# Optimization experiments

Measured on AMD Instinct MI355X. Metric: run time of the kernel, lower is better.

The kernel has to match this reference:

```python
import jax, jax.numpy as jnp
import numpy as np

# norse LIF/LI defaults
DT = 1e-3
TAU_SYN_INV = 200.0
TAU_MEM_INV = 100.0
V_TH = 1.0
V_LEAK = 0.0
V_RESET = 0.0
ALPHA = 100.0  # SuperSpike surrogate slope ('super' method)
N_CLASSES = 10


@jax.custom_vjp
def spike(x):
    # heaviside forward, SuperSpike surrogate backward
    return (x > 0).astype(x.dtype)

def _spike_fwd(x):
    return spike(x), x

def _spike_bwd(x, g):
    return (g / (ALPHA * jnp.abs(x) + 1.0) ** 2,)

spike.defvjp(_spike_fwd, _spike_bwd)


def conv2d(x, w, b):
    y = jax.lax.conv_general_dilated(x, w, (1, 1), 'VALID',
                                     dimension_numbers=('NCHW', 'OIHW', 'NCHW'))
    return y + b[None, :, None, None]


def maxpool2(x):
    return jax.lax.reduce_window(x, -jnp.inf, jax.lax.max,
                                 (1, 1, 2, 2), (1, 1, 2, 2), 'VALID')


def lif_step(inp, v, i):
    # norse lif_feed_forward_step
    v_dec = v + DT * TAU_MEM_INV * ((V_LEAK - v) + i)
    i_dec = i * (1.0 - DT * TAU_SYN_INV)
    z = spike(v_dec - V_TH)
    v_new = (1.0 - z) * v_dec + z * V_RESET
    i_new = i_dec + inp
    return z, v_new, i_new


def setup_inputs() -> dict:
    key = jax.random.key(0)
    ks = jax.random.split(key, 9)
    T, B, C, H = 32, 32, 1, 64
    feats = 13 * 13 * 32  # 5408
    return {
        'x': jax.random.normal(ks[0], (T, B, C, H, H), jnp.float32),
        'conv1_w': jax.random.normal(ks[1], (16, 1, 5, 5), jnp.float32) * 0.2,
        'conv1_b': jax.random.normal(ks[2], (16,), jnp.float32) * 0.1,
        'conv2_w': jax.random.normal(ks[3], (32, 16, 5, 5), jnp.float32) * 0.05,
        'conv2_b': jax.random.normal(ks[4], (32,), jnp.float32) * 0.1,
        'fc1_w': jax.random.normal(ks[5], (500, feats), jnp.float32) * 0.02,
        'fc1_b': jax.random.normal(ks[6], (500,), jnp.float32) * 0.1,
        'out_w': jax.random.normal(ks[7], (10, 500), jnp.float32) * 0.06,
    }


def reference(x, conv1_w, conv1_b, conv2_w, conv2_b, fc1_w, fc1_b, out_w):
    B = x.shape[1]
    zeros = lambda s: jnp.zeros(s, x.dtype)
    init = ((zeros((B, 16, 60, 60)), zeros((B, 16, 60, 60))),
            (zeros((B, 32, 26, 26)), zeros((B, 32, 26, 26))),
            (zeros((B, 500)), zeros((B, 500))),
            (zeros((B, N_CLASSES)), zeros((B, N_CLASSES))))

    def step(state, xt):
        (v0, i0), (v1, i1), (v2, i2), (vo, io) = state
        z = conv2d(xt, conv1_w, conv1_b)                     # [B,16,60,60]
        z, v0, i0 = lif_step(z, v0, i0)
        z = maxpool2(z)                                      # [B,16,30,30]
        z = N_CLASSES * conv2d(z, conv2_w, conv2_b)          # [B,32,26,26]
        z, v1, i1 = lif_step(z, v1, i1)
        z = maxpool2(z).reshape(B, -1)                       # [B,5408]
        z = z @ fc1_w.T + fc1_b                              # [B,500]
        z, v2, i2 = lif_step(z, v2, i2)
        zr = jax.nn.relu(z)
        # LI (non-spiking) linear readout cell: norse li_step, no bias
        v_out = vo + DT * TAU_MEM_INV * ((V_LEAK - vo) + io)
        io = io * (1.0 - DT * TAU_SYN_INV) + zr @ out_w.T
        return ((v0, i0), (v1, i1), (v2, i2), (v_out, io)), v_out

    _, voltages = jax.lax.scan(step, init, x)
    return voltages  # [T, B, n_classes]
```

## Files before the change

kernel.cpp:

```cpp
#include <hip/hip_runtime.h>


#define T_STEPS 32

typedef __bf16 bf16x8 __attribute__((ext_vector_type(8)));
typedef float f32x16 __attribute__((ext_vector_type(16)));
typedef int i32x4 __attribute__((ext_vector_type(4)));

__device__ __forceinline__ int xcd_swz(int orig, int nwg) {
    const int q = nwg >> 3, r = nwg & 7;
    const int xcd = orig & 7, idx = orig >> 3;
    return (xcd < r ? xcd * (q + 1) : r * (q + 1) + (xcd - r) * q) + idx;
}

__global__ __launch_bounds__(256) void k_tr(
    const float* __restrict__ x, float* __restrict__ xT)
{
    const int y = blockIdx.x, t = blockIdx.y;
    const int tid = threadIdx.x;
    __shared__ float tile[32][65];

    const int lx = tid & 63, bg = tid >> 6;
    #pragma unroll
    for (int p = 0; p < 8; ++p) {
        const int b = bg + p * 4;
        tile[b][lx] = x[((size_t)(t * 32 + b) * 64 + y) * 64 + lx];
    }
    __syncthreads();
    const int wb = tid & 31, xg = tid >> 5;
    #pragma unroll
    for (int p = 0; p < 8; ++p) {
        const int xx = xg + p * 8;
        xT[((size_t)(t * 64 + y) * 64 + xx) * 32 + wb] = tile[wb][xx];
    }
}

__global__ __launch_bounds__(256) void k1_conv1(
    const float* __restrict__ xT,
    const float* __restrict__ w1,
    const float* __restrict__ b1,
    unsigned short* __restrict__ zp1c)
{
    const int pos = xcd_swz(blockIdx.x, 900);
    const int py = pos / 30, px = pos % 30;
    const int y0 = 2 * py, x0 = 2 * px;
    const int tid = threadIdx.x;
    const int b = tid & 31, slot = tid >> 5;

    __shared__ float win2[8 * 18 * 64];

    float wreg[2][25];
    #pragma unroll
    for (int k = 0; k < 25; ++k) {
        wreg[0][k] = w1[slot * 25 + k];
        wreg[1][k] = w1[(slot + 8) * 25 + k];
    }
    const float bias0 = b1[slot], bias1 = b1[slot + 8];

    float v[2][4] = {{0.f,0.f,0.f,0.f},{0.f,0.f,0.f,0.f}};
    float cu[2][4] = {{0.f,0.f,0.f,0.f},{0.f,0.f,0.f,0.f}};

    const size_t obase = (size_t)pos * 256 + (slot >> 1) * 64 + b * 2 + (slot & 1);

    for (int tp = 0; tp < 4; ++tp) {
        __syncthreads();
        for (int i = tid; i < 1152; i += 256) {
            const int tt2 = i / 144;
            const int rem = i - tt2 * 144;
            const int p = rem >> 3, bq = rem & 7;
            const int r = p / 3, cpair = p - r * 3;
            const int b0 = bq * 4;
            const float* __restrict__ s0 = xT +
                ((size_t)((tp * 8 + tt2) * 64 + y0 + r) * 64 + (x0 + 2 * cpair)) * 32 + b0;
            const float4 v0 = *(const float4*)s0;
            const float4 v1 = *(const float4*)(s0 + 32);
            float2* __restrict__ d =
                (float2*)win2 + ((tt2 * 18 + p) * 32 + b0);
            d[0] = make_float2(v0.x, v1.x);
            d[1] = make_float2(v0.y, v1.y);
            d[2] = make_float2(v0.z, v1.z);
            d[3] = make_float2(v0.w, v1.w);
        }
        __syncthreads();

        for (int tt = 0; tt < 8; ++tt) {
            const int t = tp * 8 + tt;
            float xr[36];
            #pragma unroll
            for (int p = 0; p < 18; ++p) {
                const float2 u = ((const float2*)win2)[(tt * 18 + p) * 32 + b];
                const int r = p / 3, cpair = p - r * 3;
                xr[r * 6 + 2 * cpair]     = u.x;
                xr[r * 6 + 2 * cpair + 1] = u.y;
            }

            float acc0[4] = {0.f, 0.f, 0.f, 0.f};
            float acc1[4] = {0.f, 0.f, 0.f, 0.f};
            #pragma unroll
            for (int ky = 0; ky < 5; ++ky) {
                #pragma unroll
                for (int kx = 0; kx < 5; ++kx) {
                    const int tap = ky * 5 + kx;
                    const float e00 = xr[ky * 6 + kx];
                    const float e01 = xr[ky * 6 + kx + 1];
                    const float e10 = xr[(ky + 1) * 6 + kx];
                    const float e11 = xr[(ky + 1) * 6 + kx + 1];
                    const float w0 = wreg[0][tap];
                    acc0[0] = fmaf(w0, e00, acc0[0]);
                    acc0[1] = fmaf(w0, e01, acc0[1]);
                    acc0[2] = fmaf(w0, e10, acc0[2]);
                    acc0[3] = fmaf(w0, e11, acc0[3]);
                    const float w1v = wreg[1][tap];
                    acc1[0] = fmaf(w1v, e00, acc1[0]);
                    acc1[1] = fmaf(w1v, e01, acc1[1]);
                    acc1[2] = fmaf(w1v, e10, acc1[2]);
                    acc1[3] = fmaf(w1v, e11, acc1[3]);
                }
            }

            #pragma unroll
            for (int half = 0; half < 2; ++half) {
                const float* acc = half ? acc1 : acc0;
                const float bias = half ? bias1 : bias0;
                float zmax = 0.f;
                #pragma unroll
                for (int q = 0; q < 4; ++q) {
                    const float inp = acc[q] + bias;
                    const float vv = v[half][q], curr = cu[half][q];
                    const float vd = vv + 0.1f * (curr - vv);
                    const float id = 0.8f * curr;
                    const float z = (vd - 1.0f > 0.0f) ? 1.0f : 0.0f;
                    v[half][q] = (z > 0.f) ? 0.f : vd;
                    cu[half][q] = id + inp;
                    zmax = fmaxf(zmax, z);
                }
                zp1c[(size_t)t * 460800 + (size_t)half * 230400 + obase] =
                    (unsigned short)(__float_as_uint(zmax) >> 16);
            }
        }
    }
}

__global__ __launch_bounds__(256) void k2w_split(
    const float* __restrict__ w2, unsigned short* __restrict__ wsplit)
{
    const int i = blockIdx.x * 256 + threadIdx.x;
    if (i >= 12800) return;
    const int co = i / 400, rest = i % 400;
    const int ci = rest / 25, tap = rest % 25;
    const float w = w2[i];
    const unsigned wb = __float_as_uint(w);
    const unsigned hi = wb & 0xFFFF0000u;
    const float r1 = w - __uint_as_float(hi);
    const unsigned mid = __float_as_uint(r1) & 0xFFFF0000u;
    const float r2 = r1 - __uint_as_float(mid);
    const unsigned lo = __float_as_uint(r2) & 0xFFFF0000u;
    const int base = (tap * 32 + co) * 16 + ci;
    wsplit[base]         = (unsigned short)(hi >> 16);
    wsplit[12800 + base] = (unsigned short)(mid >> 16);
    wsplit[25600 + base] = (unsigned short)(lo >> 16);
}

__global__ __launch_bounds__(256, 2) void k2a_mfma(
    const unsigned* __restrict__ zp1c,
    const unsigned short* __restrict__ wsplit,
    float* __restrict__ raw)
{
    __shared__ i32x4 wlds[4800];
    const int tid = threadIdx.x;
    for (int i = tid; i < 4800; i += 256)
        wlds[i] = ((const i32x4*)wsplit)[i];
    __syncthreads();

    const int w = tid >> 6, l = tid & 63;
    const int task = xcd_swz(blockIdx.x, 1352) * 4 + w;
    const int t = task / 169, pg = task % 169;
    const int py = pg / 13, px = pg % 13;
    const int b = l & 31, cig = l >> 5;
    const int abase = (l & 31) * 2 + cig;

    const unsigned* __restrict__ zt =
        zp1c + (size_t)(t * 2 + cig) * 115200 + ((2 * py) * 30 + 2 * px) * 128 + b;

    f32x16 accA, accB, accC, accD;
    #pragma unroll
    for (int r = 0; r < 16; ++r) { accA[r] = 0.f; accB[r] = 0.f; accC[r] = 0.f; accD[r] = 0.f; }

    #pragma unroll
    for (int wy = 0; wy < 6; ++wy) {
        i32x4 bw[6];
        #pragma unroll
        for (int wx = 0; wx < 6; ++wx) {
            const unsigned* __restrict__ c = zt + (wy * 30 + wx) * 128;
            bw[wx][0] = (int)c[0];
            bw[wx][1] = (int)c[32];
            bw[wx][2] = (int)c[64];
            bw[wx][3] = (int)c[96];
        }
        if (wy <= 4) {
            #pragma unroll
            for (int sp = 0; sp < 3; ++sp) {
                #pragma unroll
                for (int kx = 0; kx < 5; ++kx) {
                    const int tap = wy * 5 + kx;
                    const bf16x8 A = __builtin_bit_cast(bf16x8, wlds[(sp * 25 + tap) * 64 + abase]);
                    accA = __builtin_amdgcn_mfma_f32_32x32x16_bf16(
                        A, __builtin_bit_cast(bf16x8, bw[kx]),     accA, 0, 0, 0);
                    accB = __builtin_amdgcn_mfma_f32_32x32x16_bf16(
                        A, __builtin_bit_cast(bf16x8, bw[kx + 1]), accB, 0, 0, 0);
                }
            }
        }
        if (wy >= 1) {
            #pragma unroll
            for (int sp = 0; sp < 3; ++sp) {
                #pragma unroll
                for (int kx = 0; kx < 5; ++kx) {
                    const int tap = (wy - 1) * 5 + kx;
                    const bf16x8 A = __builtin_bit_cast(bf16x8, wlds[(sp * 25 + tap) * 64 + abase]);
                    accC = __builtin_amdgcn_mfma_f32_32x32x16_bf16(
                        A, __builtin_bit_cast(bf16x8, bw[kx]),     accC, 0, 0, 0);
                    accD = __builtin_amdgcn_mfma_f32_32x32x16_bf16(
                        A, __builtin_bit_cast(bf16x8, bw[kx + 1]), accD, 0, 0, 0);
                }
            }
        }
    }

    float* __restrict__ rp = raw + (size_t)(t * 169 + pg) * 4096 + b;
    const int hi = l >> 5;
    #pragma unroll
    for (int r = 0; r < 16; ++r) {
        const int row = (r & 3) + 8 * (r >> 2) + 4 * hi;
        rp[row * 32]        = accA[r];
        rp[1024 + row * 32] = accB[r];
        rp[2048 + row * 32] = accC[r];
        rp[3072 + row * 32] = accD[r];
    }
}

__global__ __launch_bounds__(256) void k2b_lifpool(
    const float* __restrict__ raw,
    const float* __restrict__ b2,
    unsigned short* __restrict__ zb)
{
    const int bid = blockIdx.x;
    const int pg = bid >> 2, cog = bid & 3;
    const int tid = threadIdx.x;
    const int co = cog * 8 + (tid >> 5), b = tid & 31;
    const float bias = b2[co];
    const float* __restrict__ rp = raw + (size_t)pg * 4096 + co * 32 + b;

    const int k = co * 169 + pg;
    const size_t zidx0 = ((size_t)((k >> 4) * 2 + ((k >> 3) & 1)) * 32 + b) * 8 + (k & 7);

    float v0=0.f,v1=0.f,v2=0.f,v3=0.f, c0=0.f,c1=0.f,c2=0.f,c3=0.f;
    for (int t = 0; t < T_STEPS; ++t) {
        const float* __restrict__ r = rp + (size_t)t * 692224;
        float zm = 0.f;
        { const float inp = 10.f*(r[0]    + bias); const float vd = v0 + 0.1f*(c0-v0);
          const float z = (vd-1.f>0.f)?1.f:0.f; v0 = (z>0.f)?0.f:vd; c0 = 0.8f*c0 + inp;
          zm = fmaxf(zm, z); }
        { const float inp = 10.f*(r[1024] + bias); const float vd = v1 + 0.1f*(c1-v1);
          const float z = (vd-1.f>0.f)?1.f:0.f; v1 = (z>0.f)?0.f:vd; c1 = 0.8f*c1 + inp;
          zm = fmaxf(zm, z); }
        { const float inp = 10.f*(r[2048] + bias); const float vd = v2 + 0.1f*(c2-v2);
          const float z = (vd-1.f>0.f)?1.f:0.f; v2 = (z>0.f)?0.f:vd; c2 = 0.8f*c2 + inp;
          zm = fmaxf(zm, z); }
        { const float inp = 10.f*(r[3072] + bias); const float vd = v3 + 0.1f*(c3-v3);
          const float z = (vd-1.f>0.f)?1.f:0.f; v3 = (z>0.f)?0.f:vd; c3 = 0.8f*c3 + inp;
          zm = fmaxf(zm, z); }
        zb[(size_t)t * 173056 + zidx0] =
            (unsigned short)(__float_as_uint(zm) >> 16);
    }
}

__global__ __launch_bounds__(256) void k3w_split(
    const float* __restrict__ fw, unsigned short* __restrict__ wf)
{
    const int gid = blockIdx.x * 256 + threadIdx.x;
    const int l = gid & 31;
    const int ks = (gid >> 5) % 338;
    const int nt = gid / 10816;
    const int n = nt * 32 + l;

    unsigned hipk[8], midpk[8], lopk[8];
    #pragma unroll
    for (int p = 0; p < 8; ++p) {
        unsigned h[2], m[2], o[2];
        #pragma unroll
        for (int e = 0; e < 2; ++e) {
            const float w = (n < 500) ? fw[(size_t)n * 5408 + ks * 16 + 2 * p + e] : 0.f;
            const unsigned wb = __float_as_uint(w);
            const unsigned hi = wb & 0xFFFF0000u;
            const float r1 = w - __uint_as_float(hi);
            const unsigned mid = __float_as_uint(r1) & 0xFFFF0000u;
            const float r2 = r1 - __uint_as_float(mid);
            h[e] = hi >> 16; m[e] = mid >> 16; o[e] = __float_as_uint(r2) >> 16;
        }
        hipk[p]  = h[0] | (h[1] << 16);
        midpk[p] = m[0] | (m[1] << 16);
        lopk[p]  = o[0] | (o[1] << 16);
    }

    i32x4* __restrict__ wv = (i32x4*)wf;
    const int base = (nt * 338 + ks) * 64 + l * 2;
    i32x4 a, bq;
    a[0]=(int)hipk[0];a[1]=(int)hipk[1];a[2]=(int)hipk[2];a[3]=(int)hipk[3];
    bq[0]=(int)hipk[4];bq[1]=(int)hipk[5];bq[2]=(int)hipk[6];bq[3]=(int)hipk[7];
    wv[base] = a; wv[base + 1] = bq;
    a[0]=(int)midpk[0];a[1]=(int)midpk[1];a[2]=(int)midpk[2];a[3]=(int)midpk[3];
    bq[0]=(int)midpk[4];bq[1]=(int)midpk[5];bq[2]=(int)midpk[6];bq[3]=(int)midpk[7];
    wv[base + 346112] = a; wv[base + 346113] = bq;
    a[0]=(int)lopk[0];a[1]=(int)lopk[1];a[2]=(int)lopk[2];a[3]=(int)lopk[3];
    bq[0]=(int)lopk[4];bq[1]=(int)lopk[5];bq[2]=(int)lopk[6];bq[3]=(int)lopk[7];
    wv[base + 692224] = a; wv[base + 692225] = bq;
}

__global__ __launch_bounds__(256) void k3_mfma(
    const unsigned short* __restrict__ wf,
    const unsigned short* __restrict__ zb,
    float* __restrict__ part)
{
    const int wgid = xcd_swz(blockIdx.x, 416);
    const int ntg = wgid / 52, rest = wgid % 52;
    const int kc = rest >> 2, cgg = rest & 3;
    const int tid = threadIdx.x;
    const int w = tid >> 6, l = tid & 63;
    const int nt = ntg * 2 + (w >> 1);
    const int cg = cgg * 2 + (w & 1);
    const int lo5 = l & 31, hi1 = l >> 5;

    const i32x4* __restrict__ wv = (const i32x4*)wf;
    const i32x4* __restrict__ zv = (const i32x4*)zb;

    f32x16 acc0, acc1, acc2, acc3;
    #pragma unroll
    for (int r = 0; r < 16; ++r) { acc0[r]=0.f; acc1[r]=0.f; acc2[r]=0.f; acc3[r]=0.f; }

    const int ks0 = kc * 26;
    #pragma unroll 2
    for (int kk = 0; kk < 26; ++kk) {
        const int ks = ks0 + kk;
        const int ab = (nt * 338 + ks) * 64 + lo5 * 2 + hi1;
        const bf16x8 A0 = __builtin_bit_cast(bf16x8, wv[ab]);
        const bf16x8 A1 = __builtin_bit_cast(bf16x8, wv[ab + 346112]);
        const bf16x8 A2 = __builtin_bit_cast(bf16x8, wv[ab + 692224]);
        const int b0 = (((cg * 4) * 338 + ks) * 2 + hi1) * 32 + lo5;
        const bf16x8 B0 = __builtin_bit_cast(bf16x8, zv[b0]);
        const bf16x8 B1 = __builtin_bit_cast(bf16x8, zv[b0 + 21632]);
        const bf16x8 B2 = __builtin_bit_cast(bf16x8, zv[b0 + 43264]);
        const bf16x8 B3 = __builtin_bit_cast(bf16x8, zv[b0 + 64896]);
        acc0 = __builtin_amdgcn_mfma_f32_32x32x16_bf16(A0, B0, acc0, 0, 0, 0);
        acc1 = __builtin_amdgcn_mfma_f32_32x32x16_bf16(A0, B1, acc1, 0, 0, 0);
        acc2 = __builtin_amdgcn_mfma_f32_32x32x16_bf16(A0, B2, acc2, 0, 0, 0);
        acc3 = __builtin_amdgcn_mfma_f32_32x32x16_bf16(A0, B3, acc3, 0, 0, 0);
        acc0 = __builtin_amdgcn_mfma_f32_32x32x16_bf16(A1, B0, acc0, 0, 0, 0);
        acc1 = __builtin_amdgcn_mfma_f32_32x32x16_bf16(A1, B1, acc1, 0, 0, 0);
        acc2 = __builtin_amdgcn_mfma_f32_32x32x16_bf16(A1, B2, acc2, 0, 0, 0);
        acc3 = __builtin_amdgcn_mfma_f32_32x32x16_bf16(A1, B3, acc3, 0, 0, 0);
        acc0 = __builtin_amdgcn_mfma_f32_32x32x16_bf16(A2, B0, acc0, 0, 0, 0);
        acc1 = __builtin_amdgcn_mfma_f32_32x32x16_bf16(A2, B1, acc1, 0, 0, 0);
        acc2 = __builtin_amdgcn_mfma_f32_32x32x16_bf16(A2, B2, acc2, 0, 0, 0);
        acc3 = __builtin_amdgcn_mfma_f32_32x32x16_bf16(A2, B3, acc3, 0, 0, 0);
    }

    float* __restrict__ pp = part + ((size_t)(kc * 512 + nt * 32)) * 1024 + cg * 128 + lo5;
    #pragma unroll
    for (int r = 0; r < 16; ++r) {
        const int row = (r & 3) + 8 * (r >> 2) + 4 * hi1;
        pp[row * 1024]      = acc0[r];
        pp[row * 1024 + 32] = acc1[r];
        pp[row * 1024 + 64] = acc2[r];
        pp[row * 1024 + 96] = acc3[r];
    }
}

__global__ __launch_bounds__(256) void k3b_lif(
    const float* __restrict__ part,
    const float* __restrict__ fb,
    float* __restrict__ za)
{
    const int idx = blockIdx.x * 256 + threadIdx.x;
    if (idx >= 16000) return;
    const int n = idx >> 5, b = idx & 31;
    const float bias = fb[n];

    float v = 0.f, cu = 0.f;
    for (int t = 0; t < T_STEPS; ++t) {
        float s = 0.f;
        #pragma unroll
        for (int p = 0; p < 13; ++p)
            s += part[(size_t)p * 524288 + n * 1024 + t * 32 + b];
        s += bias;

        const float vd = v + 0.1f * (cu - v);
        const float id = 0.8f * cu;
        const float z = (vd - 1.0f > 0.0f) ? 1.0f : 0.0f;
        v = (z > 0.f) ? 0.f : vd;
        cu = id + s;
        za[(size_t)t * 16000 + idx] = z;
    }
}

__global__ __launch_bounds__(256) void k4_dot(
    const float* __restrict__ za,
    const float* __restrict__ ow,
    float* __restrict__ dota)
{
    const int c = blockIdx.x, t = blockIdx.y;
    const int tid = threadIdx.x;
    const int b = tid & 31, nc = tid >> 5;
    const float* __restrict__ wr = ow + c * 500;
    const float* __restrict__ zt = za + (size_t)t * 16000;

    float acc = 0.f;
    for (int j = 0; j < 63; ++j) {
        const int n = nc * 63 + j;
        if (n < 500) acc = fmaf(zt[n * 32 + b], wr[n], acc);
    }

    __shared__ float red[256];
    red[tid] = acc;
    __syncthreads();
    if (tid < 32) {
        float dot = 0.f;
        #pragma unroll
        for (int q = 0; q < 8; ++q) dot += red[q * 32 + tid];
        dota[((size_t)t * 10 + c) * 32 + tid] = dot;
    }
}

__global__ __launch_bounds__(320) void k5_li(
    const float* __restrict__ dota,
    float* __restrict__ outp)
{
    const int tid = threadIdx.x;
    if (tid >= 320) return;
    const int c = tid / 32, b = tid & 31;

    float vo = 0.f, io = 0.f;
    for (int t = 0; t < T_STEPS; ++t) {
        const float vout = vo + 0.1f * (io - vo);
        outp[t * 320 + b * 10 + c] = vout;
        vo = vout;
        io = 0.8f * io + dota[(t * 10 + c) * 32 + b];
    }
}

extern "C" void kernel_launch(void* const* d_in, const int* in_sizes, int n_in,
                              void* d_out, int out_size, void* d_ws, size_t ws_size,
                              hipStream_t stream) {
    const float* x  = (const float*)d_in[0];
    const float* w1 = (const float*)d_in[1];
    const float* b1 = (const float*)d_in[2];
    const float* w2 = (const float*)d_in[3];
    const float* b2 = (const float*)d_in[4];
    const float* fw = (const float*)d_in[5];
    const float* fb = (const float*)d_in[6];
    const float* ow = (const float*)d_in[7];
    float* out = (float*)d_out;
    float* ws = (float*)d_ws;

    size_t off = 0;
    float* zp1a = ws + off; off += 14745600;
    float* za   = ws + off; off += 512000;
    float* dota = ws + off; off += 10240;
    unsigned short* wsplit = (unsigned short*)(ws + off); off += 19200;
    float* big  = ws + off; off += 22151168;

    float* xT       = big;
    float* conv2raw = big;
    float* part     = big;
    unsigned short* zp1c16 = (unsigned short*)zp1a;
    unsigned short* zb = (unsigned short*)zp1a;
    unsigned short* wf = (unsigned short*)(zp1a + 4194304);

    k2w_split<<<50, 256, 0, stream>>>(w2, wsplit);
    k_tr     <<<dim3(64, 32), 256, 0, stream>>>(x, xT);
    k1_conv1 <<<900, 256, 0, stream>>>(xT, w1, b1, zp1c16);
    k2a_mfma <<<1352, 256, 0, stream>>>((const unsigned*)zp1c16, wsplit, conv2raw);
    k2b_lifpool<<<676, 256, 0, stream>>>(conv2raw, b2, zb);
    k3w_split<<<676, 256, 0, stream>>>(fw, wf);
    k3_mfma  <<<416, 256, 0, stream>>>(wf, zb, part);
    k3b_lif  <<<63, 256, 0, stream>>>(part, fb, za);
    k4_dot   <<<dim3(10, 32), 256, 0, stream>>>(za, ow, dota);
    k5_li    <<<1, 320, 0, stream>>>(dota, out);
}
```

Before: 216.9 us.

## Merge prep kernels into one launch and prefetch conv1 input windows

```diff
diff --git a/kernel.cpp b/kernel.cpp
--- a/kernel.cpp
+++ b/kernel.cpp
@@ -13,25 +13,85 @@
     return (xcd < r ? xcd * (q + 1) : r * (q + 1) + (xcd - r) * q) + idx;
 }
 
-__global__ __launch_bounds__(256) void k_tr(
-    const float* __restrict__ x, float* __restrict__ xT)
-{
-    const int y = blockIdx.x, t = blockIdx.y;
-    const int tid = threadIdx.x;
+__global__ __launch_bounds__(256) void k_prep(
+    const float* __restrict__ x,  float* __restrict__ xT,
+    const float* __restrict__ w2, unsigned short* __restrict__ wsplit,
+    const float* __restrict__ fw, unsigned short* __restrict__ wf)
+{
     __shared__ float tile[32][65];
-
-    const int lx = tid & 63, bg = tid >> 6;
-    #pragma unroll
-    for (int p = 0; p < 8; ++p) {
-        const int b = bg + p * 4;
-        tile[b][lx] = x[((size_t)(t * 32 + b) * 64 + y) * 64 + lx];
-    }
-    __syncthreads();
-    const int wb = tid & 31, xg = tid >> 5;
-    #pragma unroll
-    for (int p = 0; p < 8; ++p) {
-        const int xx = xg + p * 8;
-        xT[((size_t)(t * 64 + y) * 64 + xx) * 32 + wb] = tile[wb][xx];
+    const int bid = blockIdx.x;
+    const int tid = threadIdx.x;
+
+    if (bid < 2048) {
+        const int y = bid & 63, t = bid >> 6;
+        const int lx = tid & 63, bg = tid >> 6;
+        #pragma unroll
+        for (int p = 0; p < 8; ++p) {
+            const int b = bg + p * 4;
+            tile[b][lx] = x[((size_t)(t * 32 + b) * 64 + y) * 64 + lx];
+        }
+        __syncthreads();
+        const int wb = tid & 31, xg = tid >> 5;
+        #pragma unroll
+        for (int p = 0; p < 8; ++p) {
+            const int xx = xg + p * 8;
+            xT[((size_t)(t * 64 + y) * 64 + xx) * 32 + wb] = tile[wb][xx];
+        }
+    } else if (bid < 2098) {
+        const int i = (bid - 2048) * 256 + tid;
+        if (i < 12800) {
+            const int co = i / 400, rest = i % 400;
+            const int ci = rest / 25, tap = rest % 25;
+            const float w = w2[i];
+            const unsigned wb = __float_as_uint(w);
+            const unsigned hi = wb & 0xFFFF0000u;
+            const float r1 = w - __uint_as_float(hi);
+            const unsigned mid = __float_as_uint(r1) & 0xFFFF0000u;
+            const float r2 = r1 - __uint_as_float(mid);
+            const unsigned lo = __float_as_uint(r2) & 0xFFFF0000u;
+            const int base = (tap * 32 + co) * 16 + ci;
+            wsplit[base]         = (unsigned short)(hi >> 16);
+            wsplit[12800 + base] = (unsigned short)(mid >> 16);
+            wsplit[25600 + base] = (unsigned short)(lo >> 16);
+        }
+    } else {
+        const int gid = (bid - 2098) * 256 + tid;
+        const int l = gid & 31;
+        const int ks = (gid >> 5) % 338;
+        const int nt = gid / 10816;
+        const int n = nt * 32 + l;
+
+        unsigned hipk[8], midpk[8], lopk[8];
+        #pragma unroll
+        for (int p = 0; p < 8; ++p) {
+            unsigned h[2], m[2], o[2];
+            #pragma unroll
+            for (int e = 0; e < 2; ++e) {
+                const float w = (n < 500) ? fw[(size_t)n * 5408 + ks * 16 + 2 * p + e] : 0.f;
+                const unsigned wb = __float_as_uint(w);
+                const unsigned hi = wb & 0xFFFF0000u;
+                const float r1 = w - __uint_as_float(hi);
+                const unsigned mid = __float_as_uint(r1) & 0xFFFF0000u;
+                const float r2 = r1 - __uint_as_float(mid);
+                h[e] = hi >> 16; m[e] = mid >> 16; o[e] = __float_as_uint(r2) >> 16;
+            }
+            hipk[p]  = h[0] | (h[1] << 16);
+            midpk[p] = m[0] | (m[1] << 16);
+            lopk[p]  = o[0] | (o[1] << 16);
+        }
+
+        i32x4* __restrict__ wv = (i32x4*)wf;
+        const int base = (nt * 338 + ks) * 64 + l * 2;
+        i32x4 a, bq;
+        a[0]=(int)hipk[0];a[1]=(int)hipk[1];a[2]=(int)hipk[2];a[3]=(int)hipk[3];
+        bq[0]=(int)hipk[4];bq[1]=(int)hipk[5];bq[2]=(int)hipk[6];bq[3]=(int)hipk[7];
+        wv[base] = a; wv[base + 1] = bq;
+        a[0]=(int)midpk[0];a[1]=(int)midpk[1];a[2]=(int)midpk[2];a[3]=(int)midpk[3];
+        bq[0]=(int)midpk[4];bq[1]=(int)midpk[5];bq[2]=(int)midpk[6];bq[3]=(int)midpk[7];
+        wv[base + 346112] = a; wv[base + 346113] = bq;
+        a[0]=(int)lopk[0];a[1]=(int)lopk[1];a[2]=(int)lopk[2];a[3]=(int)lopk[3];
+        bq[0]=(int)lopk[4];bq[1]=(int)lopk[5];bq[2]=(int)lopk[6];bq[3]=(int)lopk[7];
+        wv[base + 692224] = a; wv[base + 692225] = bq;
     }
 }
 
@@ -62,26 +122,48 @@
 
     const size_t obase = (size_t)pos * 256 + (slot >> 1) * 64 + b * 2 + (slot & 1);
 
+    float4 pfA[5], pfB[5];
+
+#define K1_LOAD(cc)                                                          \
+    _Pragma("unroll")                                                        \
+    for (int ro = 0; ro < 5; ++ro) {                                         \
+        if (ro < 4 || tid < 128) {                                           \
+            const int i = ro * 256 + tid;                                    \
+            const int tt2 = i / 144;                                         \
+            const int rem = i - tt2 * 144;                                   \
+            const int p = rem >> 3, bq = rem & 7;                            \
+            const int r = p / 3, cpair = p - r * 3;                          \
+            const float* __restrict__ s0 = xT +                              \
+                ((size_t)(((cc) * 8 + tt2) * 64 + y0 + r) * 64 +             \
+                 (x0 + 2 * cpair)) * 32 + bq * 4;                            \
+            pfA[ro] = *(const float4*)s0;                                    \
+            pfB[ro] = *(const float4*)(s0 + 32);                             \
+        }                                                                    \
+    }
+
+#define K1_WRITE()                                                           \
+    _Pragma("unroll")                                                        \
+    for (int ro = 0; ro < 5; ++ro) {                                         \
+        if (ro < 4 || tid < 128) {                                           \
+            const int i = ro * 256 + tid;                                    \
+            const int tt2 = i / 144;                                         \
+            const int rem = i - tt2 * 144;                                   \
+            const int p = rem >> 3, bq = rem & 7;                            \
+            float2* __restrict__ d =                                         \
+                (float2*)win2 + ((tt2 * 18 + p) * 32 + bq * 4);              \
+            d[0] = make_float2(pfA[ro].x, pfB[ro].x);                        \
+            d[1] = make_float2(pfA[ro].y, pfB[ro].y);                        \
+            d[2] = make_float2(pfA[ro].z, pfB[ro].z);                        \
+            d[3] = make_float2(pfA[ro].w, pfB[ro].w);                        \
+        }                                                                    \
+    }
+
+    K1_LOAD(0);
+    K1_WRITE();
+    __syncthreads();
+
     for (int tp = 0; tp < 4; ++tp) {
-        __syncthreads();
-        for (int i = tid; i < 1152; i += 256) {
-            const int tt2 = i / 144;
-            const int rem = i - tt2 * 144;
-            const int p = rem >> 3, bq = rem & 7;
-            const int r = p / 3, cpair = p - r * 3;
-            const int b0 = bq * 4;
-            const float* __restrict__ s0 = xT +
-                ((size_t)((tp * 8 + tt2) * 64 + y0 + r) * 64 + (x0 + 2 * cpair)) * 32 + b0;
-            const float4 v0 = *(const float4*)s0;
-            const float4 v1 = *(const float4*)(s0 + 32);
-            float2* __restrict__ d =
-                (float2*)win2 + ((tt2 * 18 + p) * 32 + b0);
-            d[0] = make_float2(v0.x, v1.x);
-            d[1] = make_float2(v0.y, v1.y);
-            d[2] = make_float2(v0.z, v1.z);
-            d[3] = make_float2(v0.w, v1.w);
-        }
-        __syncthreads();
+        if (tp < 3) K1_LOAD(tp + 1);
 
         for (int tt = 0; tt < 8; ++tt) {
             const int t = tp * 8 + tt;
@@ -138,27 +220,15 @@
                     (unsigned short)(__float_as_uint(zmax) >> 16);
             }
         }
-    }
-}
-
-__global__ __launch_bounds__(256) void k2w_split(
-    const float* __restrict__ w2, unsigned short* __restrict__ wsplit)
-{
-    const int i = blockIdx.x * 256 + threadIdx.x;
-    if (i >= 12800) return;
-    const int co = i / 400, rest = i % 400;
-    const int ci = rest / 25, tap = rest % 25;
-    const float w = w2[i];
-    const unsigned wb = __float_as_uint(w);
-    const unsigned hi = wb & 0xFFFF0000u;
-    const float r1 = w - __uint_as_float(hi);
-    const unsigned mid = __float_as_uint(r1) & 0xFFFF0000u;
-    const float r2 = r1 - __uint_as_float(mid);
-    const unsigned lo = __float_as_uint(r2) & 0xFFFF0000u;
-    const int base = (tap * 32 + co) * 16 + ci;
-    wsplit[base]         = (unsigned short)(hi >> 16);
-    wsplit[12800 + base] = (unsigned short)(mid >> 16);
-    wsplit[25600 + base] = (unsigned short)(lo >> 16);
+
+        if (tp < 3) {
+            __syncthreads();
+            K1_WRITE();
+            __syncthreads();
+        }
+    }
+#undef K1_LOAD
+#undef K1_WRITE
 }
 
 __global__ __launch_bounds__(256, 2) void k2a_mfma(
@@ -273,48 +343,6 @@
         zb[(size_t)t * 173056 + zidx0] =
             (unsigned short)(__float_as_uint(zm) >> 16);
     }
-}
-
-__global__ __launch_bounds__(256) void k3w_split(
-    const float* __restrict__ fw, unsigned short* __restrict__ wf)
-{
-    const int gid = blockIdx.x * 256 + threadIdx.x;
-    const int l = gid & 31;
-    const int ks = (gid >> 5) % 338;
-    const int nt = gid / 10816;
-    const int n = nt * 32 + l;
-
-    unsigned hipk[8], midpk[8], lopk[8];
-    #pragma unroll
-    for (int p = 0; p < 8; ++p) {
-        unsigned h[2], m[2], o[2];
-        #pragma unroll
-        for (int e = 0; e < 2; ++e) {
-            const float w = (n < 500) ? fw[(size_t)n * 5408 + ks * 16 + 2 * p + e] : 0.f;
-            const unsigned wb = __float_as_uint(w);
-            const unsigned hi = wb & 0xFFFF0000u;
-            const float r1 = w - __uint_as_float(hi);
-            const unsigned mid = __float_as_uint(r1) & 0xFFFF0000u;
-            const float r2 = r1 - __uint_as_float(mid);
-            h[e] = hi >> 16; m[e] = mid >> 16; o[e] = __float_as_uint(r2) >> 16;
-        }
-        hipk[p]  = h[0] | (h[1] << 16);
-        midpk[p] = m[0] | (m[1] << 16);
-        lopk[p]  = o[0] | (o[1] << 16);
-    }
-
-    i32x4* __restrict__ wv = (i32x4*)wf;
-    const int base = (nt * 338 + ks) * 64 + l * 2;
-    i32x4 a, bq;
-    a[0]=(int)hipk[0];a[1]=(int)hipk[1];a[2]=(int)hipk[2];a[3]=(int)hipk[3];
-    bq[0]=(int)hipk[4];bq[1]=(int)hipk[5];bq[2]=(int)hipk[6];bq[3]=(int)hipk[7];
-    wv[base] = a; wv[base + 1] = bq;
-    a[0]=(int)midpk[0];a[1]=(int)midpk[1];a[2]=(int)midpk[2];a[3]=(int)midpk[3];
-    bq[0]=(int)midpk[4];bq[1]=(int)midpk[5];bq[2]=(int)midpk[6];bq[3]=(int)midpk[7];
-    wv[base + 346112] = a; wv[base + 346113] = bq;
-    a[0]=(int)lopk[0];a[1]=(int)lopk[1];a[2]=(int)lopk[2];a[3]=(int)lopk[3];
-    bq[0]=(int)lopk[4];bq[1]=(int)lopk[5];bq[2]=(int)lopk[6];bq[3]=(int)lopk[7];
-    wv[base + 692224] = a; wv[base + 692225] = bq;
 }
 
 __global__ __launch_bounds__(256) void k3_mfma(
@@ -467,6 +495,7 @@
     float* za   = ws + off; off += 512000;
     float* dota = ws + off; off += 10240;
     unsigned short* wsplit = (unsigned short*)(ws + off); off += 19200;
+    float* wfbuf = ws + off; off += 4153344;
     float* big  = ws + off; off += 22151168;
 
     float* xT       = big;
@@ -474,14 +503,12 @@
     float* part     = big;
     unsigned short* zp1c16 = (unsigned short*)zp1a;
     unsigned short* zb = (unsigned short*)zp1a;
-    unsigned short* wf = (unsigned short*)(zp1a + 4194304);
-
-    k2w_split<<<50, 256, 0, stream>>>(w2, wsplit);
-    k_tr     <<<dim3(64, 32), 256, 0, stream>>>(x, xT);
+    unsigned short* wf = (unsigned short*)wfbuf;
+
+    k_prep   <<<2774, 256, 0, stream>>>(x, xT, w2, wsplit, fw, wf);
     k1_conv1 <<<900, 256, 0, stream>>>(xT, w1, b1, zp1c16);
     k2a_mfma <<<1352, 256, 0, stream>>>((const unsigned*)zp1c16, wsplit, conv2raw);
     k2b_lifpool<<<676, 256, 0, stream>>>(conv2raw, b2, zb);
-    k3w_split<<<676, 256, 0, stream>>>(fw, wf);
     k3_mfma  <<<416, 256, 0, stream>>>(wf, zb, part);
     k3b_lif  <<<63, 256, 0, stream>>>(part, fb, za);
     k4_dot   <<<dim3(10, 32), 256, 0, stream>>>(za, ow, dota);
```

Result: slower. 236.5 us (+9.1%).
